# Kernel tuning notes

Hardware: AMD Instinct MI355X
Metric: run time of the kernel (lower is better)

## Reference

```python
import jax, jax.numpy as jnp
import numpy as np
import math

B, S, DIM = 2, 2048, 1024
N_HEADS, N_KV = 16, 4
HD = DIM // N_HEADS          # 64
N_REP = N_HEADS // N_KV      # 4
ROPE_THETA = 5000.0


def _rope_tables(seqlen, head_dim, theta):
    freqs = 1.0 / (theta ** (np.arange(0, head_dim, 2, dtype=np.float32) / head_dim))
    angles = np.outer(np.arange(seqlen, dtype=np.float32), freqs)  # [S, HD/2]
    return jnp.asarray(np.cos(angles)), jnp.asarray(np.sin(angles))


def setup_inputs() -> dict:
    key = jax.random.key(0)
    ks = jax.random.split(key, 6)
    x = jax.random.normal(ks[0], (B, S, DIM), dtype=jnp.float32)
    cos, sin = _rope_tables(S, HD, ROPE_THETA)
    # additive causal mask: 0 on/below diagonal, -inf above
    mask = jnp.where(jnp.tril(jnp.ones((S, S), dtype=bool)), 0.0, -jnp.inf).astype(jnp.float32)
    wq = jax.random.normal(ks[1], (DIM, N_HEADS * HD), dtype=jnp.float32) * 0.02
    wk = jax.random.normal(ks[2], (DIM, N_KV * HD), dtype=jnp.float32) * 0.02
    wv = jax.random.normal(ks[3], (DIM, N_KV * HD), dtype=jnp.float32) * 0.02
    wo = jax.random.normal(ks[4], (N_HEADS * HD, DIM), dtype=jnp.float32) * 0.02
    return {"x": x, "cos": cos, "sin": sin, "mask": mask,
            "wq": wq, "wk": wk, "wv": wv, "wo": wo}


def _apply_rope(t, cos, sin):
    # t: [B, S, H, HD]; even/odd interleaved pairs form complex numbers
    te, to = t[..., 0::2], t[..., 1::2]               # [B,S,H,HD/2]
    c = cos[None, :, None, :]
    s = sin[None, :, None, :]
    re = te * c - to * s
    im = te * s + to * c
    return jnp.stack([re, im], axis=-1).reshape(t.shape)  # re-interleave


def reference(x, cos, sin, mask, wq, wk, wv, wo):
    bsz, seqlen, _ = x.shape
    q = (x @ wq).reshape(bsz, seqlen, N_HEADS, HD)
    k = (x @ wk).reshape(bsz, seqlen, N_KV, HD)
    v = (x @ wv).reshape(bsz, seqlen, N_KV, HD)
    q = _apply_rope(q, cos, sin)
    k = _apply_rope(k, cos, sin)
    # GQA: group query heads as [kv_head g, rep r] instead of repeating K/V
    qg = q.reshape(bsz, seqlen, N_KV, N_REP, HD)
    scores = jnp.einsum('bsgrd,btgd->bgrst', qg, k) / math.sqrt(HD)  # [B,G,R,S,S]
    scores = scores + mask[None, None, None, :, :]
    p = jax.nn.softmax(scores, axis=-1)
    out = jnp.einsum('bgrst,btgd->bsgrd', p, v)       # [B,S,G,R,HD]
    out = out.reshape(bsz, seqlen, N_HEADS * HD)
    return out @ wo
```

## Files before the change

### kernel.cpp

```cpp
#include <hip/hip_runtime.h>
#include <math.h>

#define S_LEN 2048
#define B_SZ 2

typedef __bf16 bf16_8 __attribute__((ext_vector_type(8)));
typedef float  f32_4  __attribute__((ext_vector_type(4)));

__device__ __forceinline__ unsigned short ftob(float f) {
  union { __bf16 h; unsigned short u; } cv;
  cv.h = (__bf16)f;
  return cv.u;
}

__device__ __forceinline__ void gll16(const unsigned short* g, unsigned short* l) {
  __builtin_amdgcn_global_load_lds(
      (const __attribute__((address_space(1))) unsigned int*)g,
      (__attribute__((address_space(3))) unsigned int*)l, 16, 0, 0);
}

#define QSCALE (0.125f * 1.44269504f)


__device__ __forceinline__ void tr_tile(const float* __restrict__ W,
                                        unsigned short* __restrict__ Wt,
                                        int N, int bx, int by, float (*T)[33])
{
  const int k0 = by * 32, n0 = bx * 32;
  const int r = threadIdx.x >> 3, c4 = (threadIdx.x & 7) * 4;
  const float4 v = *(const float4*)&W[(size_t)(k0 + r) * N + n0 + c4];
  T[r][c4 + 0] = v.x; T[r][c4 + 1] = v.y;
  T[r][c4 + 2] = v.z; T[r][c4 + 3] = v.w;
  __syncthreads();
  ushort4 o;
  o.x = ftob(T[c4 + 0][r]); o.y = ftob(T[c4 + 1][r]);
  o.z = ftob(T[c4 + 2][r]); o.w = ftob(T[c4 + 3][r]);
  *(ushort4*)&Wt[(size_t)(n0 + r) * 1024 + k0 + c4] = o;
}

__global__ __launch_bounds__(256) void prep(
    const float* __restrict__ x, const float* __restrict__ wq,
    const float* __restrict__ wk, const float* __restrict__ wv,
    const float* __restrict__ wo,
    unsigned short* __restrict__ xb, unsigned short* __restrict__ wqkvt,
    unsigned short* __restrict__ wot)
{
  __shared__ float T[32][33];
  const int idx = blockIdx.x;
  if (idx < 1024) {
    tr_tile(wq, wqkvt, 1024, idx & 31, idx >> 5, T);
  } else if (idx < 1280) {
    const int i = idx - 1024;
    tr_tile(wk, wqkvt + 1024 * 1024, 256, i & 7, i >> 3, T);
  } else if (idx < 1536) {
    const int i = idx - 1280;
    tr_tile(wv, wqkvt + 1280 * 1024, 256, i & 7, i >> 3, T);
  } else if (idx < 2560) {
    const int i = idx - 1536;
    tr_tile(wo, wot, 1024, i & 31, i >> 5, T);
  } else {
    const int i = idx - 2560;
#pragma unroll
    for (int j = 0; j < 4; ++j) {
      const int id = i * 1024 + (int)threadIdx.x + j * 256;
      const float4 v = ((const float4*)x)[id];
      ushort4 o;
      o.x = ftob(v.x); o.y = ftob(v.y); o.z = ftob(v.z); o.w = ftob(v.w);
      ((ushort4*)xb)[id] = o;
    }
  }
}

#define G64DB_STAGE(A_, B_, bo_, k0_)                                           \
  do {                                                                          \
    const int r = tid >> 2, o8 = (tid & 3) * 8;                                 \
    gll16(&A_[(size_t)(bm + r) * 1024 + (k0_) + o8], &sm[(bo_) + tid * 8]);     \
    gll16(&A_[(size_t)(bm + r) * 1024 + (k0_) + 32 + o8],                       \
          &sm[(bo_) + 2048 + tid * 8]);                                         \
    gll16(&B_[(size_t)(bn0 * 128 + r) * 1024 + (k0_) + o8],                     \
          &sm[(bo_) + 4096 + tid * 8]);                                         \
    gll16(&B_[(size_t)(bn0 * 128 + r + 64) * 1024 + (k0_) + o8],                \
          &sm[(bo_) + 6144 + tid * 8]);                                         \
    gll16(&B_[(size_t)(bn0 * 128 + r) * 1024 + (k0_) + 32 + o8],                \
          &sm[(bo_) + 8192 + tid * 8]);                                         \
    gll16(&B_[(size_t)(bn0 * 128 + r + 64) * 1024 + (k0_) + 32 + o8],           \
          &sm[(bo_) + 10240 + tid * 8]);                                        \
  } while (0)

#define G64DB_KLOOP(A_, B_)                                                     \
  G64DB_STAGE(A_, B_, 0, 0);                                                    \
  __syncthreads();                                                              \
  for (int s = 0; s < 16; ++s) {                                                \
    const int bo = (s & 1) * 12288;                                             \
    if (s < 15) G64DB_STAGE(A_, B_, bo ^ 12288, (s + 1) * 64);                  \
    bf16_8 af[2][2], bf[2][4];                                                  \
    _Pragma("unroll")                                                           \
    for (int ks = 0; ks < 2; ++ks) {                                            \
      _Pragma("unroll")                                                         \
      for (int mt = 0; mt < 2; ++mt)                                            \
        af[ks][mt] = *(const bf16_8*)&sm[bo + ks * 2048 +                       \
                                         (mh + mt * 16 + l16) * 32 + quad * 8]; \
      _Pragma("unroll")                                                         \
      for (int nt = 0; nt < 4; ++nt)                                            \
        bf[ks][nt] = *(const bf16_8*)&sm[bo + 4096 + ks * 4096 +                \
                                         (nh + nt * 16 + l16) * 32 + quad * 8]; \
    }                                                                           \
    _Pragma("unroll")                                                           \
    for (int ks = 0; ks < 2; ++ks)                                              \
      _Pragma("unroll")                                                         \
      for (int mt = 0; mt < 2; ++mt)                                            \
        _Pragma("unroll")                                                       \
        for (int nt = 0; nt < 4; ++nt)                                          \
          acc[mt][nt] = __builtin_amdgcn_mfma_f32_16x16x32_bf16(                \
              af[ks][mt], bf[ks][nt], acc[mt][nt], 0, 0, 0);                    \
    __syncthreads();                                                            \
  }

__global__ __launch_bounds__(256, 3) void gemm_qkv(
    const unsigned short* __restrict__ A, const unsigned short* __restrict__ Bt,
    unsigned short* __restrict__ qb, unsigned short* __restrict__ Kimg,
    unsigned short* __restrict__ Vimg,
    const float* __restrict__ cosT, const float* __restrict__ sinT)
{
  __shared__ unsigned short sm[24576];
  const int bm = blockIdx.y * 64, bn0 = blockIdx.x;
  const int tid = threadIdx.x;
  const int w = tid >> 6, lane = tid & 63, l16 = lane & 15, quad = lane >> 4;
  const int mh = (w & 1) * 32, nh = (w >> 1) * 64;

  f32_4 acc[2][4];
#pragma unroll
  for (int mt = 0; mt < 2; ++mt)
#pragma unroll
    for (int nt = 0; nt < 4; ++nt) acc[mt][nt] = (f32_4){0.f, 0.f, 0.f, 0.f};

  G64DB_KLOOP(A, Bt);

  const int colbase = bn0 * 128;
  if (colbase < 1024) {
#pragma unroll
    for (int mt = 0; mt < 2; ++mt)
#pragma unroll
      for (int r = 0; r < 4; ++r) {
        const int row = bm + mh + mt * 16 + quad * 4 + r;
        const int s = row & (S_LEN - 1);
#pragma unroll
        for (int nt = 0; nt < 4; ++nt) {
          const int col = colbase + nh + nt * 16 + l16;
          float val = acc[mt][nt][r];
          const float pv = __shfl_xor(val, 1);
          const int fi = (col & 63) >> 1;
          const float cc = cosT[s * 32 + fi], ss = sinT[s * 32 + fi];
          val = (l16 & 1) ? fmaf(pv, ss, val * cc) : fmaf(val, cc, -(pv * ss));
          qb[(size_t)row * 1024 + col] = ftob(val * QSCALE);
        }
      }
  } else if (colbase < 1280) {
#pragma unroll
    for (int mt = 0; mt < 2; ++mt)
#pragma unroll
      for (int r = 0; r < 4; ++r) {
        const int row = bm + mh + mt * 16 + quad * 4 + r;
        const int s = row & (S_LEN - 1), bi = row >> 11;
        const int tile = s >> 6, key = s & 63;
        const int kk = key & 31, jj = kk & 7;
        const int rowp = ((key >> 5) << 5) + ((jj >> 2) << 4) + ((kk >> 3) << 2) + (jj & 3);
#pragma unroll
        for (int nt = 0; nt < 4; ++nt) {
          const int col = colbase + nh + nt * 16 + l16;
          float val = acc[mt][nt][r];
          const float pv = __shfl_xor(val, 1);
          const int fi = (col & 63) >> 1;
          const float cc = cosT[s * 32 + fi], ss = sinT[s * 32 + fi];
          val = (l16 & 1) ? fmaf(pv, ss, val * cc) : fmaf(val, cc, -(pv * ss));
          const int gcol = col - 1024, g = gcol >> 6, d = gcol & 63;
          Kimg[(size_t)((bi * 4 + g) * 32 + tile) * 4096 + rowp * 64 +
               (((d >> 3) ^ (rowp & 7)) * 8) + (d & 7)] = ftob(val);
        }
      }
  } else {
    const int bi = bm >> 11, t0 = (bm & 2047) >> 6;
    const int gp = (bn0 - 10) * 2;
    __syncthreads();
    {
      unsigned short* Ts = sm + (w >> 1) * 4608;
#pragma unroll
      for (int mt = 0; mt < 2; ++mt)
#pragma unroll
        for (int nt = 0; nt < 4; ++nt) {
          const int keyb = mh + mt * 16 + quad * 4;
          const int d = nt * 16 + l16;
          ushort4 pk;
#pragma unroll
          for (int r = 0; r < 4; ++r) ((unsigned short*)&pk)[r] = ftob(acc[mt][nt][r]);
          *(ushort4*)&Ts[d * 72 + keyb] = pk;
        }
    }
    __syncthreads();
#pragma unroll
    for (int it = 0; it < 4; ++it) {
      const int c = tid + it * 256;
      const int img = c >> 9, cc = c & 511;
      const int d = cc >> 3, ch = cc & 7;
      const uint4 v = *(const uint4*)&sm[img * 4608 + d * 72 + ch * 8];
      *(uint4*)&Vimg[(size_t)((bi * 4 + gp + img) * 32 + t0) * 4096 + d * 64 +
                     ((ch ^ (d & 7)) * 8)] = v;
    }
  }
}

__global__ __launch_bounds__(256, 2) void gemm_wo(
    const unsigned short* __restrict__ A, const unsigned short* __restrict__ Bt,
    float* __restrict__ C)
{
  __shared__ unsigned short sm[24576];
  const int bm = blockIdx.y * 64, bn0 = blockIdx.x;
  const int tid = threadIdx.x;
  const int w = tid >> 6, lane = tid & 63, l16 = lane & 15, quad = lane >> 4;
  const int mh = (w & 1) * 32, nh = (w >> 1) * 64;

  f32_4 acc[2][4];
#pragma unroll
  for (int mt = 0; mt < 2; ++mt)
#pragma unroll
    for (int nt = 0; nt < 4; ++nt) acc[mt][nt] = (f32_4){0.f, 0.f, 0.f, 0.f};

  G64DB_KLOOP(A, Bt);

#pragma unroll
  for (int mt = 0; mt < 2; ++mt)
#pragma unroll
    for (int r = 0; r < 4; ++r) {
      const int row = bm + mh + mt * 16 + quad * 4 + r;
#pragma unroll
      for (int nt = 0; nt < 4; ++nt)
        C[(size_t)row * 1024 + bn0 * 128 + nh + nt * 16 + l16] = acc[mt][nt][r];
    }
}

__global__ __launch_bounds__(512, 4) void flash_attn_v11(
    const unsigned short* __restrict__ Q, const unsigned short* __restrict__ Kimg,
    const unsigned short* __restrict__ Vimg, unsigned short* __restrict__ O)
{
  __shared__ unsigned short Ks[2][8192];
  __shared__ unsigned short Vs[2][8192];
  __shared__ float lbuf[4][2][64];
  const int id = blockIdx.x;
  const int gb = id & 7;
  const int g = gb & 3, b = gb >> 2;
  const int j = id >> 3;
  const int qc = (j < 32) ? (63 - j) : (j - 32);
  const int tid = threadIdx.x;
  const int w = tid >> 6, lane = tid & 63, l16 = lane & 15, quad = lane >> 4;
  const int hw = w & 3, par = w >> 2;
  const int h = g * 4 + hw;
  const int qbase = qc * 32;
  const int swz = l16 & 7;

  union { bf16_8 v; unsigned short u[8]; } ones;
#pragma unroll
  for (int i = 0; i < 8; ++i) ones.u[i] = 0x3f80;

  bf16_8 bq[2][2];
#pragma unroll
  for (int qf = 0; qf < 2; ++qf) {
    const unsigned short* qp =
        Q + ((size_t)(b * S_LEN + qbase + qf * 16 + l16)) * 1024 + h * 64;
    bq[qf][0] = *(const bf16_8*)(qp + quad * 8);
    bq[qf][1] = *(const bf16_8*)(qp + 32 + quad * 8);
  }

  f32_4 acc[2][4], acc_l[2];
#pragma unroll
  for (int qf = 0; qf < 2; ++qf) {
    acc_l[qf] = (f32_4){0.f, 0.f, 0.f, 0.f};
#pragma unroll
    for (int mt = 0; mt < 4; ++mt) acc[qf][mt] = (f32_4){0.f, 0.f, 0.f, 0.f};
  }

  const unsigned short* kim = Kimg + (size_t)(gb * 32) * 4096;
  const unsigned short* vim = Vimg + (size_t)(gb * 32) * 4096;
  const int ntiles = (qc >> 1) + 1;
  const int steps = (ntiles + 1) >> 1;
  const int hq = (qc & 1) * 32;

  {
    gll16(kim + tid * 8, &Ks[0][tid * 8]);
    gll16(kim + (tid + 512) * 8, &Ks[0][(tid + 512) * 8]);
    gll16(vim + tid * 8, &Vs[0][tid * 8]);
    gll16(vim + (tid + 512) * 8, &Vs[0][(tid + 512) * 8]);
  }
  for (int s = 0; s < steps; ++s) {
    const int c = s & 1;
    __syncthreads();
    if (s + 1 < steps) {
      const unsigned short* kp = kim + (size_t)(s + 1) * 8192;
      const unsigned short* vp = vim + (size_t)(s + 1) * 8192;
      gll16(kp + tid * 8, &Ks[c ^ 1][tid * 8]);
      gll16(kp + (tid + 512) * 8, &Ks[c ^ 1][(tid + 512) * 8]);
      gll16(vp + tid * 8, &Vs[c ^ 1][tid * 8]);
      gll16(vp + (tid + 512) * 8, &Vs[c ^ 1][(tid + 512) * 8]);
    }

    const int tile = 2 * s + par;
    if (tile < ntiles) {
      const bool diag = (tile == ntiles - 1);
      const unsigned short* ks = &Ks[c][par * 4096];
      const unsigned short* vs = &Vs[c][par * 4096];
      union { bf16_8 v; unsigned int wd[4]; } pf[2][2];
#pragma unroll
      for (int mt = 0; mt < 4; ++mt) {
        const int krow = (mt * 16 + l16) * 64;
        const bf16_8 kf0 = *(const bf16_8*)&ks[krow + (quad ^ swz) * 8];
        const bf16_8 kf1 = *(const bf16_8*)&ks[krow + ((4 + quad) ^ swz) * 8];
#pragma unroll
        for (int qf = 0; qf < 2; ++qf) {
          f32_4 z = (f32_4){0.f, 0.f, 0.f, 0.f};
          __builtin_amdgcn_s_setprio(1);
          z = __builtin_amdgcn_mfma_f32_16x16x32_bf16(kf0, bq[qf][0], z, 0, 0, 0);
          z = __builtin_amdgcn_mfma_f32_16x16x32_bf16(kf1, bq[qf][1], z, 0, 0, 0);
          __builtin_amdgcn_s_setprio(0);
          float pv[4];
#pragma unroll
          for (int r = 0; r < 4; ++r) {
            float p = __builtin_amdgcn_exp2f(z[r]);
            if (diag) {
              const int keyl = ((mt >> 1) << 5) + quad * 8 + ((mt & 1) << 2) + r;
              const int ql = hq + qf * 16 + l16;
              p = (keyl > ql) ? 0.f : p;
            }
            pv[r] = p;
          }
          pf[qf][mt >> 1].wd[(mt & 1) * 2 + 0] =
              (unsigned int)ftob(pv[0]) | ((unsigned int)ftob(pv[1]) << 16);
          pf[qf][mt >> 1].wd[(mt & 1) * 2 + 1] =
              (unsigned int)ftob(pv[2]) | ((unsigned int)ftob(pv[3]) << 16);
        }
      }
#pragma unroll
      for (int qf = 0; qf < 2; ++qf) {
        acc_l[qf] = __builtin_amdgcn_mfma_f32_16x16x32_bf16(ones.v, pf[qf][0].v, acc_l[qf], 0, 0, 0);
        acc_l[qf] = __builtin_amdgcn_mfma_f32_16x16x32_bf16(ones.v, pf[qf][1].v, acc_l[qf], 0, 0, 0);
      }
      __builtin_amdgcn_s_setprio(1);
#pragma unroll
      for (int mt = 0; mt < 4; ++mt) {
        const int vrow = (mt * 16 + l16) * 64;
        const bf16_8 vf0 = *(const bf16_8*)&vs[vrow + (quad ^ swz) * 8];
        const bf16_8 vf1 = *(const bf16_8*)&vs[vrow + ((4 + quad) ^ swz) * 8];
#pragma unroll
        for (int qf = 0; qf < 2; ++qf) {
          acc[qf][mt] = __builtin_amdgcn_mfma_f32_16x16x32_bf16(vf0, pf[qf][0].v, acc[qf][mt], 0, 0, 0);
          acc[qf][mt] = __builtin_amdgcn_mfma_f32_16x16x32_bf16(vf1, pf[qf][1].v, acc[qf][mt], 0, 0, 0);
        }
      }
      __builtin_amdgcn_s_setprio(0);
    }
  }

  __syncthreads();
  float* cb = (float*)&Ks[0][0];
  if (par == 1) {
    float* dst = cb + hw * 2048;
#pragma unroll
    for (int qf = 0; qf < 2; ++qf)
#pragma unroll
      for (int mt = 0; mt < 4; ++mt)
#pragma unroll
        for (int r = 0; r < 4; ++r)
          dst[(qf * 16 + mt * 4 + r) * 64 + lane] = acc[qf][mt][r];
    lbuf[hw][0][lane] = acc_l[0][0];
    lbuf[hw][1][lane] = acc_l[1][0];
  }
  __syncthreads();
  if (par == 0) {
    const float* src = cb + hw * 2048;
#pragma unroll
    for (int qf = 0; qf < 2; ++qf)
#pragma unroll
      for (int mt = 0; mt < 4; ++mt)
#pragma unroll
        for (int r = 0; r < 4; ++r)
          acc[qf][mt][r] += src[(qf * 16 + mt * 4 + r) * 64 + lane];

#pragma unroll
    for (int qf = 0; qf < 2; ++qf) {
      const float l = acc_l[qf][0] + lbuf[hw][qf][lane];
      const float inv = 1.f / l;
      unsigned short* op =
          O + ((size_t)(b * S_LEN + qbase + qf * 16 + l16)) * 1024 + h * 64;
#pragma unroll
      for (int mt = 0; mt < 4; ++mt) {
        ushort4 ov;
#pragma unroll
        for (int r = 0; r < 4; ++r) ((unsigned short*)&ov)[r] = ftob(acc[qf][mt][r] * inv);
        *(ushort4*)&op[mt * 16 + quad * 4] = ov;
      }
    }
  }
}

extern "C" void kernel_launch(void* const* d_in, const int* in_sizes, int n_in,
                              void* d_out, int out_size, void* d_ws, size_t ws_size,
                              hipStream_t stream)
{
  const float* x    = (const float*)d_in[0];
  const float* cosT = (const float*)d_in[1];
  const float* sinT = (const float*)d_in[2];
  const float* wq   = (const float*)d_in[4];
  const float* wk   = (const float*)d_in[5];
  const float* wv   = (const float*)d_in[6];
  const float* wo   = (const float*)d_in[7];
  float* out = (float*)d_out;

  char* ws = (char*)d_ws;
  const size_t MB = 1024 * 1024;
  unsigned short* xb    = (unsigned short*)(ws);
  unsigned short* qb    = (unsigned short*)(ws + 8 * MB);
  unsigned short* wqkvt = (unsigned short*)(ws + 16 * MB);
  unsigned short* Kimg  = (unsigned short*)(ws + 19 * MB);
  unsigned short* Vimg  = (unsigned short*)(ws + 21 * MB);
  unsigned short* wot   = (unsigned short*)(ws + 23 * MB);

  prep<<<3584, 256, 0, stream>>>(x, wq, wk, wv, wo, xb, wqkvt, wot);
  gemm_qkv<<<dim3(12, 64), 256, 0, stream>>>(xb, wqkvt, qb, Kimg, Vimg, cosT, sinT);
  flash_attn_v11<<<512, 512, 0, stream>>>(qb, Kimg, Vimg, qb);
  gemm_wo<<<dim3(8, 64), 256, 0, stream>>>(qb, wot, out);
}
```

Measured before the change: 167.0 us.

## Split attention KV tiles across four wave groups and sum row totals in VALU

```diff
diff --git a/kernel.cpp b/kernel.cpp
--- a/kernel.cpp
+++ b/kernel.cpp
@@ -238,28 +238,23 @@
     }
 }
 
-__global__ __launch_bounds__(512, 4) void flash_attn_v11(
+__global__ __launch_bounds__(1024, 4) void flash_attn_v12(
     const unsigned short* __restrict__ Q, const unsigned short* __restrict__ Kimg,
     const unsigned short* __restrict__ Vimg, unsigned short* __restrict__ O)
 {
-  __shared__ unsigned short Ks[2][8192];
-  __shared__ unsigned short Vs[2][8192];
-  __shared__ float lbuf[4][2][64];
+  __shared__ unsigned short KV[2][32768];
+  __shared__ float lbuf[12][2][64];
   const int id = blockIdx.x;
   const int gb = id & 7;
   const int g = gb & 3, b = gb >> 2;
-  const int j = id >> 3;
-  const int qc = (j < 32) ? (63 - j) : (j - 32);
+  const int i = id >> 3;
+  const int qc = (i < 32) ? (32 + i) : (63 - i);
   const int tid = threadIdx.x;
   const int w = tid >> 6, lane = tid & 63, l16 = lane & 15, quad = lane >> 4;
-  const int hw = w & 3, par = w >> 2;
+  const int hw = w & 3, p = w >> 2;
   const int h = g * 4 + hw;
   const int qbase = qc * 32;
   const int swz = l16 & 7;
-
-  union { bf16_8 v; unsigned short u[8]; } ones;
-#pragma unroll
-  for (int i = 0; i < 8; ++i) ones.u[i] = 0x3f80;
 
   bf16_8 bq[2][2];
 #pragma unroll
@@ -270,43 +265,40 @@
     bq[qf][1] = *(const bf16_8*)(qp + 32 + quad * 8);
   }
 
-  f32_4 acc[2][4], acc_l[2];
-#pragma unroll
-  for (int qf = 0; qf < 2; ++qf) {
-    acc_l[qf] = (f32_4){0.f, 0.f, 0.f, 0.f};
+  f32_4 acc[2][4];
+  float l_part[2] = {0.f, 0.f};
+#pragma unroll
+  for (int qf = 0; qf < 2; ++qf)
 #pragma unroll
     for (int mt = 0; mt < 4; ++mt) acc[qf][mt] = (f32_4){0.f, 0.f, 0.f, 0.f};
-  }
 
   const unsigned short* kim = Kimg + (size_t)(gb * 32) * 4096;
   const unsigned short* vim = Vimg + (size_t)(gb * 32) * 4096;
   const int ntiles = (qc >> 1) + 1;
-  const int steps = (ntiles + 1) >> 1;
+  const int steps = (ntiles + 3) >> 2;
   const int hq = (qc & 1) * 32;
 
-  {
-    gll16(kim + tid * 8, &Ks[0][tid * 8]);
-    gll16(kim + (tid + 512) * 8, &Ks[0][(tid + 512) * 8]);
-    gll16(vim + tid * 8, &Vs[0][tid * 8]);
-    gll16(vim + (tid + 512) * 8, &Vs[0][(tid + 512) * 8]);
-  }
+#define FA12_STAGE(s_, c_)                                                      \
+  do {                                                                          \
+    const unsigned short* kp = kim + (size_t)(s_) * 16384;                      \
+    const unsigned short* vp = vim + (size_t)(s_) * 16384;                      \
+    gll16(kp + tid * 8, &KV[c_][tid * 8]);                                      \
+    gll16(kp + (tid + 1024) * 8, &KV[c_][(tid + 1024) * 8]);                    \
+    gll16(vp + tid * 8, &KV[c_][16384 + tid * 8]);                              \
+    gll16(vp + (tid + 1024) * 8, &KV[c_][16384 + (tid + 1024) * 8]);            \
+  } while (0)
+
+  FA12_STAGE(0, 0);
   for (int s = 0; s < steps; ++s) {
     const int c = s & 1;
     __syncthreads();
-    if (s + 1 < steps) {
-      const unsigned short* kp = kim + (size_t)(s + 1) * 8192;
-      const unsigned short* vp = vim + (size_t)(s + 1) * 8192;
-      gll16(kp + tid * 8, &Ks[c ^ 1][tid * 8]);
-      gll16(kp + (tid + 512) * 8, &Ks[c ^ 1][(tid + 512) * 8]);
-      gll16(vp + tid * 8, &Vs[c ^ 1][tid * 8]);
-      gll16(vp + (tid + 512) * 8, &Vs[c ^ 1][(tid + 512) * 8]);
-    }
-
-    const int tile = 2 * s + par;
+    if (s + 1 < steps) FA12_STAGE(s + 1, c ^ 1);
+
+    const int tile = 4 * s + p;
     if (tile < ntiles) {
       const bool diag = (tile == ntiles - 1);
-      const unsigned short* ks = &Ks[c][par * 4096];
-      const unsigned short* vs = &Vs[c][par * 4096];
+      const unsigned short* ks = &KV[c][p * 4096];
+      const unsigned short* vs = &KV[c][16384 + p * 4096];
       union { bf16_8 v; unsigned int wd[4]; } pf[2][2];
 #pragma unroll
       for (int mt = 0; mt < 4; ++mt) {
@@ -323,13 +315,14 @@
           float pv[4];
 #pragma unroll
           for (int r = 0; r < 4; ++r) {
-            float p = __builtin_amdgcn_exp2f(z[r]);
+            float pe = __builtin_amdgcn_exp2f(z[r]);
             if (diag) {
               const int keyl = ((mt >> 1) << 5) + quad * 8 + ((mt & 1) << 2) + r;
               const int ql = hq + qf * 16 + l16;
-              p = (keyl > ql) ? 0.f : p;
+              pe = (keyl > ql) ? 0.f : pe;
             }
-            pv[r] = p;
+            l_part[qf] += pe;
+            pv[r] = pe;
           }
           pf[qf][mt >> 1].wd[(mt & 1) * 2 + 0] =
               (unsigned int)ftob(pv[0]) | ((unsigned int)ftob(pv[1]) << 16);
@@ -337,11 +330,6 @@
               (unsigned int)ftob(pv[2]) | ((unsigned int)ftob(pv[3]) << 16);
         }
       }
-#pragma unroll
-      for (int qf = 0; qf < 2; ++qf) {
-        acc_l[qf] = __builtin_amdgcn_mfma_f32_16x16x32_bf16(ones.v, pf[qf][0].v, acc_l[qf], 0, 0, 0);
-        acc_l[qf] = __builtin_amdgcn_mfma_f32_16x16x32_bf16(ones.v, pf[qf][1].v, acc_l[qf], 0, 0, 0);
-      }
       __builtin_amdgcn_s_setprio(1);
 #pragma unroll
       for (int mt = 0; mt < 4; ++mt) {
@@ -359,9 +347,10 @@
   }
 
   __syncthreads();
-  float* cb = (float*)&Ks[0][0];
-  if (par == 1) {
-    float* dst = cb + hw * 2048;
+  float* cb = (float*)&KV[0][0];
+  if (p != 0) {
+    const int slot = (p - 1) * 4 + hw;
+    float* dst = cb + slot * 2048;
 #pragma unroll
     for (int qf = 0; qf < 2; ++qf)
 #pragma unroll
@@ -369,23 +358,31 @@
 #pragma unroll
         for (int r = 0; r < 4; ++r)
           dst[(qf * 16 + mt * 4 + r) * 64 + lane] = acc[qf][mt][r];
-    lbuf[hw][0][lane] = acc_l[0][0];
-    lbuf[hw][1][lane] = acc_l[1][0];
+    lbuf[slot][0][lane] = l_part[0];
+    lbuf[slot][1][lane] = l_part[1];
   }
   __syncthreads();
-  if (par == 0) {
-    const float* src = cb + hw * 2048;
-#pragma unroll
-    for (int qf = 0; qf < 2; ++qf)
-#pragma unroll
-      for (int mt = 0; mt < 4; ++mt)
-#pragma unroll
-        for (int r = 0; r < 4; ++r)
-          acc[qf][mt][r] += src[(qf * 16 + mt * 4 + r) * 64 + lane];
+  if (p == 0) {
+#pragma unroll
+    for (int pp = 0; pp < 3; ++pp) {
+      const int slot = pp * 4 + hw;
+      const float* src = cb + slot * 2048;
+#pragma unroll
+      for (int qf = 0; qf < 2; ++qf)
+#pragma unroll
+        for (int mt = 0; mt < 4; ++mt)
+#pragma unroll
+          for (int r = 0; r < 4; ++r)
+            acc[qf][mt][r] += src[(qf * 16 + mt * 4 + r) * 64 + lane];
+      l_part[0] += lbuf[slot][0][lane];
+      l_part[1] += lbuf[slot][1][lane];
+    }
 
 #pragma unroll
     for (int qf = 0; qf < 2; ++qf) {
-      const float l = acc_l[qf][0] + lbuf[hw][qf][lane];
+      float l = l_part[qf];
+      l += __shfl_xor(l, 16);
+      l += __shfl_xor(l, 32);
       const float inv = 1.f / l;
       unsigned short* op =
           O + ((size_t)(b * S_LEN + qbase + qf * 16 + l16)) * 1024 + h * 64;
@@ -424,6 +421,6 @@
 
   prep<<<3584, 256, 0, stream>>>(x, wq, wk, wv, wo, xb, wqkvt, wot);
   gemm_qkv<<<dim3(12, 64), 256, 0, stream>>>(xb, wqkvt, qb, Kimg, Vimg, cosT, sinT);
-  flash_attn_v11<<<512, 512, 0, stream>>>(qb, Kimg, Vimg, qb);
+  flash_attn_v12<<<512, 1024, 0, stream>>>(qb, Kimg, Vimg, qb);
   gemm_wo<<<dim3(8, 64), 256, 0, stream>>>(qb, wot, out);
 }
```

After: 165.6 us. Within noise of the previous version (-0.8%).
